# Optimization experiments

Measured on AMD Instinct MI355X. Metric: run time of the kernel, lower is better.

The kernel has to match this reference:

```python
import jax, jax.numpy as jnp
import numpy as np
from jax import lax

D_MODEL = 60
D_INNER = 120   # expand=2
D_STATE = 16
D_CONV = 4
DT_RANK = 4     # ceil(60/16)
DEPTH = 2
BATCH = 2
H_IMG = 128
W_IMG = 128
L_SEQ = H_IMG * W_IMG


def setup_inputs() -> dict:
    key = jax.random.key(0)
    ks = jax.random.split(key, 12)
    s = 0.02
    x = jax.random.normal(ks[0], (BATCH, L_SEQ, D_MODEL), jnp.float32)
    ln_w = jnp.ones((DEPTH, D_MODEL), jnp.float32)
    ln_b = jnp.zeros((DEPTH, D_MODEL), jnp.float32)
    in_proj_w = jax.random.normal(ks[1], (DEPTH, 2 * D_INNER, D_MODEL), jnp.float32) * s
    conv_w = jax.random.normal(ks[2], (DEPTH, D_INNER, D_CONV), jnp.float32) * s
    conv_b = jnp.zeros((DEPTH, D_INNER), jnp.float32)
    x_proj_w = jax.random.normal(ks[3], (DEPTH, DT_RANK + 2 * D_STATE, D_INNER), jnp.float32) * s
    dt_proj_w = jax.random.normal(ks[4], (DEPTH, D_INNER, DT_RANK), jnp.float32) * s
    dt_proj_b = jnp.full((DEPTH, D_INNER), -4.0, jnp.float32)  # softplus^-1 of small dt
    A_log = jnp.broadcast_to(
        jnp.log(jnp.arange(1, D_STATE + 1, dtype=jnp.float32))[None, None, :],
        (DEPTH, D_INNER, D_STATE)).copy()
    D_skip = jnp.ones((DEPTH, D_INNER), jnp.float32)
    out_proj_w = jax.random.normal(ks[5], (DEPTH, D_MODEL, D_INNER), jnp.float32) * s
    conv2d_w = jax.random.normal(ks[6], (D_MODEL, D_MODEL, 3, 3), jnp.float32) * s
    conv2d_b = jnp.zeros((D_MODEL,), jnp.float32)
    return {"x": x, "ln_w": ln_w, "ln_b": ln_b, "in_proj_w": in_proj_w,
            "conv_w": conv_w, "conv_b": conv_b, "x_proj_w": x_proj_w,
            "dt_proj_w": dt_proj_w, "dt_proj_b": dt_proj_b, "A_log": A_log,
            "D": D_skip, "out_proj_w": out_proj_w,
            "conv2d_w": conv2d_w, "conv2d_b": conv2d_b,
            "H": H_IMG, "W": W_IMG}


def _layernorm(x, w, b, eps=1e-5):
    mu = jnp.mean(x, axis=-1, keepdims=True)
    var = jnp.mean(jnp.square(x - mu), axis=-1, keepdims=True)
    return (x - mu) * lax.rsqrt(var + eps) * w + b


def _selective_scan(dA, dBx, C):
    # dA, dBx: [B, L, D_INNER, D_STATE]; C: [B, L, D_STATE]
    def step(h, inp):
        dA_t, dBx_t, c_t = inp
        h = dA_t * h + dBx_t                       # [B, D_INNER, D_STATE]
        y = jnp.einsum('bdn,bn->bd', h, c_t)
        return h, y
    h0 = jnp.zeros(dA.shape[:1] + dA.shape[2:], dA.dtype)
    _, ys = lax.scan(step, h0,
                     (dA.transpose(1, 0, 2, 3), dBx.transpose(1, 0, 2, 3),
                      C.transpose(1, 0, 2)))
    return ys.transpose(1, 0, 2)                    # [B, L, D_INNER]


def _mamba(x, in_w, cw, cb, xp_w, dtw, dtb, A_log, D_skip, out_w):
    # x: [B, L, D_MODEL]
    xz = jnp.einsum('bld,ed->ble', x, in_w)         # [B, L, 2*D_INNER]
    xin, z = jnp.split(xz, 2, axis=-1)
    # causal depthwise conv1d over L
    xc = xin.transpose(0, 2, 1)                     # [B, D_INNER, L]
    xc = jnp.pad(xc, ((0, 0), (0, 0), (D_CONV - 1, 0)))
    xc = lax.conv_general_dilated(xc, cw[:, None, :], (1,), 'VALID',
                                  dimension_numbers=('NCH', 'OIH', 'NCH'),
                                  feature_group_count=D_INNER)
    xc = jax.nn.silu(xc + cb[None, :, None]).transpose(0, 2, 1)  # [B, L, D_INNER]
    xdb = jnp.einsum('bld,ed->ble', xc, xp_w)       # [B, L, DT_RANK + 2*D_STATE]
    dt = xdb[..., :DT_RANK]
    Bm = xdb[..., DT_RANK:DT_RANK + D_STATE]
    Cm = xdb[..., DT_RANK + D_STATE:]
    delta = jax.nn.softplus(jnp.einsum('blr,dr->bld', dt, dtw) + dtb)  # [B, L, D_INNER]
    A = -jnp.exp(A_log)                              # [D_INNER, D_STATE]
    dA = jnp.exp(delta[..., None] * A[None, None])   # [B, L, D_INNER, D_STATE]
    dBx = delta[..., None] * Bm[:, :, None, :] * xc[..., None]
    y = _selective_scan(dA, dBx, Cm) + D_skip * xc
    y = y * jax.nn.silu(z)
    return jnp.einsum('ble,de->bld', y, out_w)       # [B, L, D_MODEL]


def reference(x, ln_w, ln_b, in_proj_w, conv_w, conv_b, x_proj_w,
              dt_proj_w, dt_proj_b, A_log, D, out_proj_w,
              conv2d_w, conv2d_b, H, W):
    h = x
    for i in range(DEPTH):
        hn = _layernorm(h, ln_w[i], ln_b[i])
        h = _mamba(hn, in_proj_w[i], conv_w[i], conv_b[i], x_proj_w[i],
                   dt_proj_w[i], dt_proj_b[i], A_log[i], D[i], out_proj_w[i])
    # patch_unembed -> 3x3 conv -> patch_embed, residual add (RMMB)
    b = h.shape[0]
    img = h.transpose(0, 2, 1).reshape(b, D_MODEL, H, W)
    img = lax.conv_general_dilated(img, conv2d_w, (1, 1), 'SAME',
                                   dimension_numbers=('NCHW', 'OIHW', 'NCHW'))
    img = img + conv2d_b[None, :, None, None]
    h = img.reshape(b, D_MODEL, H * W).transpose(0, 2, 1)
    return h + x
```

## Files before the change

kernel.cpp:

```cpp
#include <hip/hip_runtime.h>
#include <math.h>

#define BATCH 2
#define LSEQ 16384
#define DM 60
#define DI 120
#define NCH 512
#define TCH 32
#define HH 128
#define WW 128

typedef __attribute__((ext_vector_type(8))) short bhalf8;
typedef __attribute__((ext_vector_type(4))) short short4v;
typedef __attribute__((ext_vector_type(4))) float f32x4;

__device__ __forceinline__ float sigmoidf_(float x){ return __builtin_amdgcn_rcpf(1.0f + __expf(-x)); }
__device__ __forceinline__ float siluf_(float x){ return x * sigmoidf_(x); }
__device__ __forceinline__ float softplusf_(float x){ return (x > 20.0f) ? x : __logf(1.0f + __expf(x)); }
__device__ __forceinline__ short f2b(float f){
  union{float f; unsigned u;} v; v.f = f;
  unsigned r = (v.u + 0x7fffu + ((v.u >> 16) & 1u)) >> 16;
  return (short)r;
}
__device__ __forceinline__ float b2f(short s){
  union{float f; unsigned u;} v; v.u = ((unsigned)(unsigned short)s) << 16; return v.f;
}

__device__ __forceinline__ void powers16(float r, float* dA){
  dA[0] = r;
  #pragma unroll
  for (int n = 1; n < 16; n++) dA[n] = dA[(n-1)>>1] * dA[n>>1];
}
__device__ __forceinline__ void powers8(float r, float* p){
  p[0] = r;
  #pragma unroll
  for (int n = 1; n < 8; n++) p[n] = p[(n-1)>>1] * p[n>>1];
}

__global__ __launch_bounds__(256) void k_pack(
    const float* __restrict__ ipw, const float* __restrict__ xpw,
    const float* __restrict__ opw,
    const float* __restrict__ lnw, const float* __restrict__ lnb,
    short* __restrict__ pk, float* __restrict__ c01)
{
  int i = blockIdx.x*256 + threadIdx.x;
  if (i < 2*240*64){
    int l = i / (240*64);
    int rem = i % (240*64);
    int n = rem / 64, k = rem % 64;
    float v = (k < 60) ? ipw[(size_t)l*14400 + n*60 + k] * lnw[l*60 + k] : 0.f;
    pk[i] = f2b(v);
  } else if (i < 30720 + 2*48*128){
    int j = i - 30720;
    int l = j / (48*128);
    int rem = j % (48*128);
    int n = rem / 128, k = rem % 128;
    float v = (n < 36 && k < 120) ? xpw[(size_t)l*36*120 + n*120 + k] : 0.f;
    pk[i] = f2b(v);
  } else if (i < 43008 + 480){
    int j = i - 43008;
    int l = j / 240, n = j % 240;
    float c1 = 0.f, c0 = 0.f;
    for (int k = 0; k < 60; k++){
      float w = ipw[(size_t)l*14400 + n*60 + k];
      c1 += lnw[l*60+k] * w;
      c0 += lnb[l*60+k] * w;
    }
    c01[(l*240 + n)*2 + 0] = c1;
    c01[(l*240 + n)*2 + 1] = c0;
  } else if (i < 43488 + 2*64*128){
    int j = i - 43488;
    int l = j / 8192;
    int rem = j % 8192;
    int n = rem / 128, k = rem % 128;
    float v = (n < 60 && k < 120) ? opw[(size_t)l*7200 + n*120 + k] : 0.f;
    pk[43008 + j] = f2b(v);
  }
}

__global__ __launch_bounds__(512) void k_lnxp(
    const float* __restrict__ srcf, const short* __restrict__ srcb,
    const short* __restrict__ ipB,
    const float* __restrict__ c01,
    const float* __restrict__ cw, const float* __restrict__ cb,
    const short* __restrict__ xpB,
    const float* __restrict__ dtw, const float* __restrict__ dtb,
    const float* __restrict__ A_log,
    short* __restrict__ zs, short* __restrict__ xcg,
    short* __restrict__ delta, short* __restrict__ BCg,
    float* __restrict__ ap, float* __restrict__ he)
{
  __shared__ __align__(16) char smem[31552];
  short* XB   = (short*)smem;
  short* xcB  = (short*)smem;
  short* xinB = (short*)(smem + 8704);
  short* delL = (short*)(smem + 8704);
  float* BLf  = (float*)(smem + 21760);
  short* BCL  = (short*)(smem + 23808);
  float* stats= (float*)(smem + 25856);
  float* dtsh = (float*)(smem + 26240);
  float* cwL  = (float*)(smem + 26752);
  float* Wd5T = (float*)(smem + 28672);
  float* cbL  = (float*)(smem + 30592);
  float* bdL  = (float*)(smem + 31072);
  const int tid = threadIdx.x;
  const int wave = tid >> 6, lane = tid & 63;
  const int m = lane & 15, quad = lane >> 4;
  const int row0 = blockIdx.x * 32;
  const int seq0 = (row0 / LSEQ) * LSEQ;
  if (tid < 480){ cwL[tid] = cw[tid]; Wd5T[(tid & 3)*120 + (tid >> 2)] = dtw[tid]; }
  if (tid < 120){ cbL[tid] = cb[tid]; bdL[tid] = dtb[tid]; }
  for (int i = tid; i < 48*16; i += 512){
    int r = i >> 4, g = i & 15;
    int grow = row0 - 3 + r;
    short4v o = {0,0,0,0};
    if (g < 15 && r < 35 && grow >= seq0){
      if (srcb){
        o = *(const short4v*)&srcb[(size_t)grow*60 + g*4];
      } else {
        float4 f = *(const float4*)&srcf[(size_t)grow*60 + g*4];
        o.x = f2b(f.x); o.y = f2b(f.y); o.z = f2b(f.z); o.w = f2b(f.w);
      }
    }
    *(short4v*)&XB[r*72 + g*4] = o;
  }
  __syncthreads();
  {
    const int sub = lane >> 4;
    const int li  = lane & 15;
    #pragma unroll
    for (int it = 0; it < 2; it++){
      int r = it*32 + wave*4 + sub;
      if (r < 48){
        short4v x4 = *(const short4v*)&XB[r*72 + li*4];
        float f0 = b2f(x4.x), f1 = b2f(x4.y), f2 = b2f(x4.z), f3 = b2f(x4.w);
        float sx = (f0 + f1) + (f2 + f3);
        float sq = (f0*f0 + f1*f1) + (f2*f2 + f3*f3);
        #pragma unroll
        for (int off = 1; off < 16; off <<= 1){
          sx += __shfl_xor(sx, off);
          sq += __shfl_xor(sq, off);
        }
        if (li == 0){
          float mu = sx * (1.0f/60.0f);
          float var = fmaxf(sq * (1.0f/60.0f) - mu*mu, 0.f);
          stats[r*2 + 0] = mu;
          stats[r*2 + 1] = rsqrtf(var + 1e-5f);
        }
      }
    }
  }
  __syncthreads();
  for (int t = wave; t < 45; t += 8){
    int mtile = t / 15, ntile = t % 15;
    f32x4 acc = {0.f,0.f,0.f,0.f};
    #pragma unroll
    for (int ks = 0; ks < 2; ks++){
      bhalf8 a = *(const bhalf8*)&XB[(mtile*16 + m)*72 + ks*32 + quad*8];
      bhalf8 b = *(const bhalf8*)&ipB[(ntile*16 + m)*64 + ks*32 + quad*8];
      acc = __builtin_amdgcn_mfma_f32_16x16x32_bf16(a, b, acc, 0, 0, 0);
    }
    int n = ntile*16 + m;
    float2 cc = *(const float2*)&c01[n*2];
    float c1v = cc.x, c0v = cc.y;
    #pragma unroll
    for (int reg = 0; reg < 4; reg++){
      int r = mtile*16 + quad*4 + reg;
      int grow = row0 - 3 + r;
      bool valid = (r < 35) && (grow >= seq0);
      float mu = stats[r*2], rs = stats[r*2+1];
      float val = rs*(acc[reg] - mu*c1v) + c0v;
      if (!valid) val = 0.f;
      if (n < 120){
        xinB[r*136 + n] = f2b(val);
      } else if (r >= 3 && r < 35){
        zs[(size_t)(row0 - 3 + r)*120 + (n - 120)] = f2b(siluf_(val));
      }
    }
  }
  __syncthreads();
  for (int i = tid; i < 960; i += 512){
    int r = i/30, c4 = (i%30)*4;
    float4 cbv = *(const float4*)&cbL[c4];
    float4 w0 = *(const float4*)&cwL[(c4+0)*4];
    float4 w1 = *(const float4*)&cwL[(c4+1)*4];
    float4 w2 = *(const float4*)&cwL[(c4+2)*4];
    float4 w3 = *(const float4*)&cwL[(c4+3)*4];
    short4v x0 = *(const short4v*)&xinB[(r+0)*136 + c4];
    short4v x1 = *(const short4v*)&xinB[(r+1)*136 + c4];
    short4v x2 = *(const short4v*)&xinB[(r+2)*136 + c4];
    short4v x3 = *(const short4v*)&xinB[(r+3)*136 + c4];
    float a0 = cbv.x + w0.x*b2f(x0.x) + w0.y*b2f(x1.x) + w0.z*b2f(x2.x) + w0.w*b2f(x3.x);
    float a1 = cbv.y + w1.x*b2f(x0.y) + w1.y*b2f(x1.y) + w1.z*b2f(x2.y) + w1.w*b2f(x3.y);
    float a2 = cbv.z + w2.x*b2f(x0.z) + w2.y*b2f(x1.z) + w2.z*b2f(x2.z) + w2.w*b2f(x3.z);
    float a3 = cbv.w + w3.x*b2f(x0.w) + w3.y*b2f(x1.w) + w3.z*b2f(x2.w) + w3.w*b2f(x3.w);
    short4v o;
    o.x = f2b(siluf_(a0)); o.y = f2b(siluf_(a1)); o.z = f2b(siluf_(a2)); o.w = f2b(siluf_(a3));
    *(short4v*)&xcB[r*136 + c4] = o;
  }
  for (int i = tid; i < 32*8; i += 512)
    xcB[(i >> 3)*136 + 120 + (i & 7)] = 0;
  __syncthreads();
  for (int t = wave; t < 6; t += 8){
    int mtile = t / 3, ntile = t % 3;
    f32x4 acc = {0.f,0.f,0.f,0.f};
    #pragma unroll
    for (int ks = 0; ks < 4; ks++){
      bhalf8 a = *(const bhalf8*)&xcB[(mtile*16 + m)*136 + ks*32 + quad*8];
      bhalf8 b = *(const bhalf8*)&xpB[(ntile*16 + m)*128 + ks*32 + quad*8];
      acc = __builtin_amdgcn_mfma_f32_16x16x32_bf16(a, b, acc, 0, 0, 0);
    }
    int n = ntile*16 + m;
    #pragma unroll
    for (int reg = 0; reg < 4; reg++){
      int r = mtile*16 + quad*4 + reg;
      float val = acc[reg];
      if (n < 4)        dtsh[r*4 + n] = val;
      else if (n < 36){
        BCL[r*32 + (n - 4)] = f2b(val);
        if (n < 20) BLf[r*16 + (n - 4)] = val;
      }
    }
  }
  __syncthreads();
  for (int i = tid; i < 960; i += 512){
    int row = i/30, c4 = (i%30)*4;
    float4 t4 = *(const float4*)&dtsh[row*4];
    float4 w0 = *(const float4*)&Wd5T[0*120 + c4];
    float4 w1 = *(const float4*)&Wd5T[1*120 + c4];
    float4 w2 = *(const float4*)&Wd5T[2*120 + c4];
    float4 w3 = *(const float4*)&Wd5T[3*120 + c4];
    float4 bb = *(const float4*)&bdL[c4];
    short4v o;
    o.x = f2b(softplusf_(bb.x + t4.x*w0.x + t4.y*w1.x + t4.z*w2.x + t4.w*w3.x));
    o.y = f2b(softplusf_(bb.y + t4.x*w0.y + t4.y*w1.y + t4.z*w2.y + t4.w*w3.y));
    o.z = f2b(softplusf_(bb.z + t4.x*w0.z + t4.y*w1.z + t4.z*w2.z + t4.w*w3.z));
    o.w = f2b(softplusf_(bb.w + t4.x*w0.w + t4.y*w1.w + t4.z*w2.w + t4.w*w3.w));
    *(short4v*)&delL[row*120 + c4] = o;
    *(short4v*)&delta[(size_t)(row0 + row)*120 + c4] = o;
  }
  __syncthreads();
  for (int i = tid; i < 960; i += 512){
    int r = i/30, off = (i%30)*4;
    *(short4v*)&xcg[(size_t)(row0 + r)*120 + off] = *(const short4v*)&xcB[r*136 + off];
  }
  for (int i = tid; i < 256; i += 512)
    *(short4v*)&BCg[(size_t)row0*32 + i*4] = *(const short4v*)&BCL[i*4];
  if (tid < 480){
    const int d = tid >> 2, q = tid & 3, n0 = q << 2;
    const int b = row0 / LSEQ;
    const int cglob = (row0 % LSEQ) >> 5;
    float A2[4], h[4];
    const float A20 = -__expf(A_log[d*16]) * 1.44269504f;
    #pragma unroll
    for (int n = 0; n < 4; n++){
      A2[n] = -__expf(A_log[d*16 + n0 + n]) * 1.44269504f;
      h[n] = 0.f;
    }
    bool fastp = true;
    #pragma unroll
    for (int n = 0; n < 4; n++)
      fastp = fastp && (fabsf(A2[n] - (n0+n+1)*A20) <= 1e-4f*fabsf(A2[n]));
    int fp = fastp ? 1 : 0;
    fp &= __shfl_xor(fp, 1);
    fp &= __shfl_xor(fp, 2);
    int base = (cglob*BATCH + b)*(DI*16) + d*16 + n0;
    if (fp){
      float P = 1.f;
      const int sh1 = q & 1, sh2 = q & 2;
      for (int t = 0; t < 32; t++){
        float del = b2f(delL[t*120 + d]);
        float xcv = b2f(xcB[t*136 + d]);
        float dx = del * xcv;
        float r = exp2f(del * A20);
        P *= r;
        float p1 = r*r;
        float p2 = p1*r, p3 = p1*p1;
        float s = sh1 ? p3 : 1.0f;
        if (sh2) s *= p3*p3;
        float4 bv = *(const float4*)&BLf[t*16 + n0];
        h[0] = (s*r )*h[0] + dx*bv.x;
        h[1] = (s*p1)*h[1] + dx*bv.y;
        h[2] = (s*p2)*h[2] + dx*bv.z;
        h[3] = (s*p3)*h[3] + dx*bv.w;
      }
      float P1 = P*P;
      float P2 = P1*P, P3 = P1*P1;
      float sP = sh1 ? P3 : 1.0f;
      if (sh2) sP *= P3*P3;
      float apv[4] = {sP*P, sP*P1, sP*P2, sP*P3};
      *(float4*)&ap[base] = *(float4*)&apv[0];
      *(float4*)&he[base] = *(float4*)&h[0];
    } else {
      float apv[4] = {1.f,1.f,1.f,1.f};
      for (int t = 0; t < 32; t++){
        float del = b2f(delL[t*120 + d]);
        float dx = del * b2f(xcB[t*136 + d]);
        #pragma unroll
        for (int n = 0; n < 4; n++){
          float dA = exp2f(del * A2[n]);
          apv[n] *= dA;
          h[n] = dA*h[n] + dx*BLf[t*16 + n0 + n];
        }
      }
      *(float4*)&ap[base] = *(float4*)&apv[0];
      *(float4*)&he[base] = *(float4*)&h[0];
    }
  }
}

__global__ __launch_bounds__(256) void k_scan2(float* __restrict__ ap, const float* __restrict__ he)
{
  __shared__ float aggA[16*17];
  __shared__ float aggB[16*17];
  const int tid = threadIdx.x;
  const int n = tid & 15, j = tid >> 4;
  const int sbase = blockIdx.x*16 + n;
  const int stride = BATCH*DI*16;
  {
    float A = 1.f, B = 0.f;
    int idx = (j*32)*stride + sbase;
    #pragma unroll 4
    for (int k = 0; k < 32; k++){
      float a = ap[idx], h = he[idx];
      B = a*B + h;
      A *= a;
      idx += stride;
    }
    aggA[n*17 + j] = A;
    aggB[n*17 + j] = B;
  }
  __syncthreads();
  if (tid < 16){
    float B = 0.f;
    #pragma unroll
    for (int jj = 0; jj < 16; jj++){
      float Af = aggA[tid*17 + jj];
      float Bf = aggB[tid*17 + jj];
      aggB[tid*17 + jj] = B;
      B = Af*B + Bf;
    }
  }
  __syncthreads();
  {
    float H = aggB[n*17 + j];
    int idx = (j*32)*stride + sbase;
    #pragma unroll 4
    for (int k = 0; k < 32; k++){
      float a = ap[idx], h = he[idx];
      ap[idx] = H;
      H = a*H + h;
      idx += stride;
    }
  }
}

__global__ __launch_bounds__(256) void k_scan3o(
    const short* __restrict__ delta, const short* __restrict__ xc,
    const short* __restrict__ BCg, const short* __restrict__ zs,
    const float* __restrict__ h0, const float* __restrict__ A_log,
    const float* __restrict__ Dsk, const short* __restrict__ opB,
    short* __restrict__ hout)
{
  __shared__ float BCl[TCH*32];
  __shared__ __align__(16) short yL[TCH*136];
  const int tid = threadIdx.x;
  const int wave = tid >> 6, lane = tid & 63;
  const int m = lane & 15, quad = lane >> 4;
  const int c = blockIdx.x % NCH, b = blockIdx.x / NCH;
  const size_t rowbase = (size_t)b*LSEQ + (size_t)c*TCH;
  for (int i = tid; i < TCH*8; i += 256){
    short4v v = *(const short4v*)&BCg[rowbase*32 + i*4];
    float4 f; f.x = b2f(v.x); f.y = b2f(v.y); f.z = b2f(v.z); f.w = b2f(v.w);
    *(float4*)&BCl[i*4] = f;
  }
  for (int i = tid; i < TCH*4; i += 256){
    short4v z = {0,0,0,0};
    *(short4v*)&yL[(i >> 2)*136 + 120 + (i & 3)*4] = z;
  }
  __syncthreads();
  if (tid < 240){
    const int d = tid >> 1, half = tid & 1, n0 = half << 3;
    float A2[8], h[8];
    const int base = (c*BATCH + b)*(DI*16) + d*16 + n0;
    const float A20 = -__expf(A_log[d*16]) * 1.44269504f;
    #pragma unroll
    for (int n = 0; n < 8; n++){
      A2[n] = -__expf(A_log[d*16 + n0 + n]) * 1.44269504f;
      h[n] = h0[base + n];
    }
    bool fastp = true;
    #pragma unroll
    for (int n = 0; n < 8; n++)
      fastp = fastp && (fabsf(A2[n] - (n0+n+1)*A20) <= 1e-4f*fabsf(A2[n]));
    int fp = fastp ? 1 : 0;
    fp &= __shfl_xor(fp, 1);
    const float Dv = Dsk[d];
    if (fp){
      for (int t = 0; t < TCH; t++){
        float del = b2f(delta[(rowbase+t)*DI + d]);
        float xcv = b2f(xc[(rowbase+t)*DI + d]);
        float zv  = b2f(zs[(rowbase+t)*DI + d]);
        float dx = del * xcv;
        float r = exp2f(del * A20);
        float p8[8]; powers8(r, p8);
        float s = half ? p8[7] : 1.0f;
        float4 b0 = *(const float4*)&BCl[t*32 + n0];
        float4 b1 = *(const float4*)&BCl[t*32 + n0 + 4];
        h[0] = (s*p8[0])*h[0] + dx*b0.x;  h[1] = (s*p8[1])*h[1] + dx*b0.y;
        h[2] = (s*p8[2])*h[2] + dx*b0.z;  h[3] = (s*p8[3])*h[3] + dx*b0.w;
        h[4] = (s*p8[4])*h[4] + dx*b1.x;  h[5] = (s*p8[5])*h[5] + dx*b1.y;
        h[6] = (s*p8[6])*h[6] + dx*b1.z;  h[7] = (s*p8[7])*h[7] + dx*b1.w;
        float4 c0 = *(const float4*)&BCl[t*32 + 16 + n0];
        float4 c1 = *(const float4*)&BCl[t*32 + 20 + n0];
        float acc = h[0]*c0.x + h[1]*c0.y + h[2]*c0.z + h[3]*c0.w
                  + h[4]*c1.x + h[5]*c1.y + h[6]*c1.z + h[7]*c1.w;
        acc += __shfl_xor(acc, 1);
        if (!half) yL[t*136 + d] = f2b((acc + Dv*xcv) * zv);
      }
    } else {
      for (int t = 0; t < TCH; t++){
        float del = b2f(delta[(rowbase+t)*DI + d]);
        float xcv = b2f(xc[(rowbase+t)*DI + d]);
        float zv  = b2f(zs[(rowbase+t)*DI + d]);
        float dx = del * xcv;
        float acc = 0.f;
        #pragma unroll
        for (int n = 0; n < 8; n++){
          float dA = exp2f(del * A2[n]);
          h[n] = dA*h[n] + dx*BCl[t*32 + n0 + n];
          acc += h[n]*BCl[t*32 + 16 + n0 + n];
        }
        acc += __shfl_xor(acc, 1);
        if (!half) yL[t*136 + d] = f2b((acc + Dv*xcv) * zv);
      }
    }
  }
  __syncthreads();
  for (int t = wave; t < 8; t += 4){
    const int mtile = t >> 2, ntile = t & 3;
    f32x4 acc = {0.f,0.f,0.f,0.f};
    #pragma unroll
    for (int ks = 0; ks < 4; ks++){
      bhalf8 a  = *(const bhalf8*)&yL[(mtile*16 + m)*136 + ks*32 + quad*8];
      bhalf8 bb = *(const bhalf8*)&opB[(ntile*16 + m)*128 + ks*32 + quad*8];
      acc = __builtin_amdgcn_mfma_f32_16x16x32_bf16(a, bb, acc, 0, 0, 0);
    }
    const int n = ntile*16 + m;
    if (n < 60){
      #pragma unroll
      for (int reg = 0; reg < 4; reg++){
        int r = mtile*16 + quad*4 + reg;
        hout[(rowbase + r)*60 + n] = f2b(acc[reg]);
      }
    }
  }
}

__global__ __launch_bounds__(256) void k_wB(const float* __restrict__ w, short* __restrict__ wB)
{
  int i = blockIdx.x*256 + threadIdx.x;
  if (i >= 9*64*64) return;
  int ci = i & 63, co = (i >> 6) & 63, tap = i >> 12;
  float v = 0.f;
  if (co < 60 && ci < 60) v = w[((size_t)co*60 + ci)*9 + tap];
  wB[i] = f2b(v);
}

__global__ __launch_bounds__(256) void k_conv2d(
    const short* __restrict__ hin, const short* __restrict__ wB,
    const float* __restrict__ cb, const float* __restrict__ xres,
    float* __restrict__ out)
{
  __shared__ short tile[3*66*72];
  const int tid = threadIdx.x;
  const int blk = blockIdx.x;
  const int xhalf = blk & 1;
  const int yy = (blk >> 1) & 127;
  const int b = blk >> 8;
  const int x0 = xhalf*64;
  for (int i = tid; i < 3*66*18; i += 256){
    int g = i % 18;
    int xx = (i / 18) % 66;
    int row = i / (18*66);
    int gy = yy - 1 + row, gx = x0 - 1 + xx;
    short4v v = {0,0,0,0};
    if (g < 15 && gy >= 0 && gy < HH && gx >= 0 && gx < WW)
      v = *(const short4v*)&hin[((size_t)b*LSEQ + gy*WW + gx)*60 + g*4];
    *(short4v*)&tile[(row*66 + xx)*72 + g*4] = v;
  }
  __syncthreads();
  const int wave = tid >> 6, lane = tid & 63;
  const int m = lane & 15, quad = lane >> 4;
  f32x4 acc0 = {0.f,0.f,0.f,0.f}, acc1 = {0.f,0.f,0.f,0.f};
  f32x4 acc2 = {0.f,0.f,0.f,0.f}, acc3 = {0.f,0.f,0.f,0.f};
  #pragma unroll
  for (int tap = 0; tap < 9; tap++){
    const int ky = tap/3, kx = tap%3;
    const short* arow = &tile[(ky*66 + wave*16 + m + kx)*72];
    const short* brow = wB + tap*4096;
    #pragma unroll
    for (int kh = 0; kh < 2; kh++){
      const int k0 = kh*32 + quad*8;
      bhalf8 a = *(const bhalf8*)(arow + k0);
      bhalf8 b0 = *(const bhalf8*)(brow + (0*16 + m)*64 + k0);
      bhalf8 b1 = *(const bhalf8*)(brow + (1*16 + m)*64 + k0);
      bhalf8 b2 = *(const bhalf8*)(brow + (2*16 + m)*64 + k0);
      bhalf8 b3 = *(const bhalf8*)(brow + (3*16 + m)*64 + k0);
      acc0 = __builtin_amdgcn_mfma_f32_16x16x32_bf16(a, b0, acc0, 0, 0, 0);
      acc1 = __builtin_amdgcn_mfma_f32_16x16x32_bf16(a, b1, acc1, 0, 0, 0);
      acc2 = __builtin_amdgcn_mfma_f32_16x16x32_bf16(a, b2, acc2, 0, 0, 0);
      acc3 = __builtin_amdgcn_mfma_f32_16x16x32_bf16(a, b3, acc3, 0, 0, 0);
    }
  }
  const size_t rowb = (size_t)b*LSEQ + yy*WW + x0;
  f32x4 accs[4] = {acc0, acc1, acc2, acc3};
  #pragma unroll
  for (int nt = 0; nt < 4; nt++){
    int co = nt*16 + m;
    if (co < 60){
      float bias = cb[co];
      #pragma unroll
      for (int reg = 0; reg < 4; reg++){
        int px = wave*16 + quad*4 + reg;
        size_t o = (rowb + px)*60 + co;
        out[o] = accs[nt][reg] + bias + xres[o];
      }
    }
  }
}

extern "C" void kernel_launch(void* const* d_in, const int* in_sizes, int n_in,
                              void* d_out, int out_size, void* d_ws, size_t ws_size,
                              hipStream_t stream)
{
  const float* x      = (const float*)d_in[0];
  const float* ln_w   = (const float*)d_in[1];
  const float* ln_b   = (const float*)d_in[2];
  const float* ipw    = (const float*)d_in[3];
  const float* cw     = (const float*)d_in[4];
  const float* cb1    = (const float*)d_in[5];
  const float* xpw    = (const float*)d_in[6];
  const float* dtw    = (const float*)d_in[7];
  const float* dtb    = (const float*)d_in[8];
  const float* A_log  = (const float*)d_in[9];
  const float* Dsk    = (const float*)d_in[10];
  const float* opw    = (const float*)d_in[11];
  const float* c2w    = (const float*)d_in[12];
  const float* c2b    = (const float*)d_in[13];
  float* out = (float*)d_out;

  char* ws = (char*)d_ws;
  size_t off = 0;
  short* zsb   = (short*)(ws + off); off += (size_t)BATCH*LSEQ*DI*2;
  short* xcb   = (short*)(ws + off); off += (size_t)BATCH*LSEQ*DI*2;
  short* dlt   = (short*)(ws + off); off += (size_t)BATCH*LSEQ*DI*2;
  short* BCg   = (short*)(ws + off); off += (size_t)BATCH*LSEQ*32*2;
  float* apb   = (float*)(ws + off); off += (size_t)NCH*BATCH*DI*16*4;
  float* heb   = (float*)(ws + off); off += (size_t)NCH*BATCH*DI*16*4;
  short* hcur  = (short*)(ws + off); off += (size_t)BATCH*LSEQ*DM*2;
  short* wBb   = (short*)(ws + off); off += (size_t)9*64*64*2;
  short* pkb   = (short*)(ws + off); off += (size_t)(2*240*64 + 2*48*128 + 2*64*128)*2;
  float* c01b  = (float*)(ws + off); off += (size_t)2*240*2*4;

  const int rows = BATCH*LSEQ;
  k_pack<<<(43008 + 480 + 16384 + 255)/256, 256, 0, stream>>>(ipw, xpw, opw, ln_w, ln_b, pkb, c01b);
  for (int layer = 0; layer < 2; layer++){
    const float* srcf = (layer == 0) ? x : nullptr;
    const short* srcb = (layer == 0) ? nullptr : hcur;
    k_lnxp<<<rows/32, 512, 0, stream>>>(srcf, srcb,
                                        pkb + (size_t)layer*240*64,
                                        c01b + (size_t)layer*240*2,
                                        cw + layer*DI*4, cb1 + layer*DI,
                                        pkb + 30720 + (size_t)layer*48*128,
                                        dtw + (size_t)layer*DI*4, dtb + layer*DI,
                                        A_log + (size_t)layer*DI*16,
                                        zsb, xcb, dlt, BCg, apb, heb);
    k_scan2<<<BATCH*DI, 256, 0, stream>>>(apb, heb);
    k_scan3o<<<BATCH*NCH, 256, 0, stream>>>(dlt, xcb, BCg, zsb, apb, A_log + (size_t)layer*DI*16,
                                            Dsk + layer*DI, pkb + 43008 + (size_t)layer*8192, hcur);
  }
  k_wB<<<(9*64*64+255)/256, 256, 0, stream>>>(c2w, wBb);
  k_conv2d<<<BATCH*HH*2, 256, 0, stream>>>(hcur, wBb, c2b, x, out);
}
```

Baseline: 277.6 us.

## Stage scan inputs in LDS and unroll chunk-state scan two steps

In k_scan3o, delta, xc and z for the chunk are now loaded cooperatively with vectorized loads into shared memory before the sequential scan. Previously each scan step issued scattered 2-byte global loads. In k_lnxp, fp32 copies of delta and the convolved x are kept in LDS so the chunk-state pass skips bf16 conversions. That pass is also unrolled by two timesteps, combining decays to shorten the dependent chain. This grows LDS usage (k_lnxp to about 48KB), which may lower occupancy.

```diff
diff --git a/kernel.cpp b/kernel.cpp
--- a/kernel.cpp
+++ b/kernel.cpp
@@ -26,11 +26,6 @@
   union{float f; unsigned u;} v; v.u = ((unsigned)(unsigned short)s) << 16; return v.f;
 }
 
-__device__ __forceinline__ void powers16(float r, float* dA){
-  dA[0] = r;
-  #pragma unroll
-  for (int n = 1; n < 16; n++) dA[n] = dA[(n-1)>>1] * dA[n>>1];
-}
 __device__ __forceinline__ void powers8(float r, float* p){
   p[0] = r;
   #pragma unroll
@@ -90,19 +85,20 @@
     short* __restrict__ delta, short* __restrict__ BCg,
     float* __restrict__ ap, float* __restrict__ he)
 {
-  __shared__ __align__(16) char smem[31552];
+  __shared__ __align__(16) char smem[49216];
   short* XB   = (short*)smem;
   short* xcB  = (short*)smem;
   short* xinB = (short*)(smem + 8704);
-  short* delL = (short*)(smem + 8704);
-  float* BLf  = (float*)(smem + 21760);
-  short* BCL  = (short*)(smem + 23808);
-  float* stats= (float*)(smem + 25856);
-  float* dtsh = (float*)(smem + 26240);
-  float* cwL  = (float*)(smem + 26752);
-  float* Wd5T = (float*)(smem + 28672);
-  float* cbL  = (float*)(smem + 30592);
-  float* bdL  = (float*)(smem + 31072);
+  float* delLf= (float*)(smem + 8704);
+  float* xcf  = (float*)(smem + 24064);
+  float* BLf  = (float*)(smem + 39424);
+  short* BCL  = (short*)(smem + 41472);
+  float* stats= (float*)(smem + 43520);
+  float* dtsh = (float*)(smem + 43904);
+  float* cwL  = (float*)(smem + 44416);
+  float* Wd5T = (float*)(smem + 46336);
+  float* cbL  = (float*)(smem + 48256);
+  float* bdL  = (float*)(smem + 48736);
   const int tid = threadIdx.x;
   const int wave = tid >> 6, lane = tid & 63;
   const int m = lane & 15, quad = lane >> 4;
@@ -194,8 +190,11 @@
     float a1 = cbv.y + w1.x*b2f(x0.y) + w1.y*b2f(x1.y) + w1.z*b2f(x2.y) + w1.w*b2f(x3.y);
     float a2 = cbv.z + w2.x*b2f(x0.z) + w2.y*b2f(x1.z) + w2.z*b2f(x2.z) + w2.w*b2f(x3.z);
     float a3 = cbv.w + w3.x*b2f(x0.w) + w3.y*b2f(x1.w) + w3.z*b2f(x2.w) + w3.w*b2f(x3.w);
+    a0 = siluf_(a0); a1 = siluf_(a1); a2 = siluf_(a2); a3 = siluf_(a3);
+    float4 fo; fo.x = a0; fo.y = a1; fo.z = a2; fo.w = a3;
+    *(float4*)&xcf[r*120 + c4] = fo;
     short4v o;
-    o.x = f2b(siluf_(a0)); o.y = f2b(siluf_(a1)); o.z = f2b(siluf_(a2)); o.w = f2b(siluf_(a3));
+    o.x = f2b(a0); o.y = f2b(a1); o.z = f2b(a2); o.w = f2b(a3);
     *(short4v*)&xcB[r*136 + c4] = o;
   }
   for (int i = tid; i < 32*8; i += 512)
@@ -231,12 +230,14 @@
     float4 w2 = *(const float4*)&Wd5T[2*120 + c4];
     float4 w3 = *(const float4*)&Wd5T[3*120 + c4];
     float4 bb = *(const float4*)&bdL[c4];
+    float4 dd;
+    dd.x = softplusf_(bb.x + t4.x*w0.x + t4.y*w1.x + t4.z*w2.x + t4.w*w3.x);
+    dd.y = softplusf_(bb.y + t4.x*w0.y + t4.y*w1.y + t4.z*w2.y + t4.w*w3.y);
+    dd.z = softplusf_(bb.z + t4.x*w0.z + t4.y*w1.z + t4.z*w2.z + t4.w*w3.z);
+    dd.w = softplusf_(bb.w + t4.x*w0.w + t4.y*w1.w + t4.z*w2.w + t4.w*w3.w);
+    *(float4*)&delLf[row*120 + c4] = dd;
     short4v o;
-    o.x = f2b(softplusf_(bb.x + t4.x*w0.x + t4.y*w1.x + t4.z*w2.x + t4.w*w3.x));
-    o.y = f2b(softplusf_(bb.y + t4.x*w0.y + t4.y*w1.y + t4.z*w2.y + t4.w*w3.y));
-    o.z = f2b(softplusf_(bb.z + t4.x*w0.z + t4.y*w1.z + t4.z*w2.z + t4.w*w3.z));
-    o.w = f2b(softplusf_(bb.w + t4.x*w0.w + t4.y*w1.w + t4.z*w2.w + t4.w*w3.w));
-    *(short4v*)&delL[row*120 + c4] = o;
+    o.x = f2b(dd.x); o.y = f2b(dd.y); o.z = f2b(dd.z); o.w = f2b(dd.w);
     *(short4v*)&delta[(size_t)(row0 + row)*120 + c4] = o;
   }
   __syncthreads();
@@ -264,25 +265,31 @@
     int fp = fastp ? 1 : 0;
     fp &= __shfl_xor(fp, 1);
     fp &= __shfl_xor(fp, 2);
+    const int sh1 = q & 1, sh2 = q & 2;
     int base = (cglob*BATCH + b)*(DI*16) + d*16 + n0;
     if (fp){
       float P = 1.f;
-      const int sh1 = q & 1, sh2 = q & 2;
-      for (int t = 0; t < 32; t++){
-        float del = b2f(delL[t*120 + d]);
-        float xcv = b2f(xcB[t*136 + d]);
-        float dx = del * xcv;
-        float r = exp2f(del * A20);
-        P *= r;
-        float p1 = r*r;
-        float p2 = p1*r, p3 = p1*p1;
-        float s = sh1 ? p3 : 1.0f;
-        if (sh2) s *= p3*p3;
-        float4 bv = *(const float4*)&BLf[t*16 + n0];
-        h[0] = (s*r )*h[0] + dx*bv.x;
-        h[1] = (s*p1)*h[1] + dx*bv.y;
-        h[2] = (s*p2)*h[2] + dx*bv.z;
-        h[3] = (s*p3)*h[3] + dx*bv.w;
+      for (int t = 0; t < 32; t += 2){
+        float d1 = delLf[t*120 + d],     d2 = delLf[(t+1)*120 + d];
+        float x1 = xcf[t*120 + d],       x2 = xcf[(t+1)*120 + d];
+        float dx1 = d1*x1, dx2 = d2*x2;
+        float r2s = exp2f(d2*A20);
+        float rr  = exp2f((d1+d2)*A20);
+        P *= rr;
+        float c1 = rr*rr, c2 = c1*rr, c3 = c1*c1;
+        float sc = sh1 ? c3 : 1.0f; if (sh2) sc *= c3*c3;
+        float p1 = r2s*r2s, p2 = p1*r2s, p3 = p1*p1;
+        float s2 = sh1 ? p3 : 1.0f; if (sh2) s2 *= p3*p3;
+        float4 b1 = *(const float4*)&BLf[t*16 + n0];
+        float4 b2 = *(const float4*)&BLf[(t+1)*16 + n0];
+        float ad0 = (s2*r2s)*dx1*b1.x + dx2*b2.x;
+        float ad1 = (s2*p1 )*dx1*b1.y + dx2*b2.y;
+        float ad2 = (s2*p2 )*dx1*b1.z + dx2*b2.z;
+        float ad3 = (s2*p3 )*dx1*b1.w + dx2*b2.w;
+        h[0] = (sc*rr)*h[0] + ad0;
+        h[1] = (sc*c1)*h[1] + ad1;
+        h[2] = (sc*c2)*h[2] + ad2;
+        h[3] = (sc*c3)*h[3] + ad3;
       }
       float P1 = P*P;
       float P2 = P1*P, P3 = P1*P1;
@@ -294,8 +301,8 @@
     } else {
       float apv[4] = {1.f,1.f,1.f,1.f};
       for (int t = 0; t < 32; t++){
-        float del = b2f(delL[t*120 + d]);
-        float dx = del * b2f(xcB[t*136 + d]);
+        float del = delLf[t*120 + d];
+        float dx = del * xcf[t*120 + d];
         #pragma unroll
         for (int n = 0; n < 4; n++){
           float dA = exp2f(del * A2[n]);
@@ -364,11 +371,20 @@
 {
   __shared__ float BCl[TCH*32];
   __shared__ __align__(16) short yL[TCH*136];
+  __shared__ __align__(16) short dL[TCH*120];
+  __shared__ __align__(16) short xL[TCH*120];
+  __shared__ __align__(16) short zL[TCH*120];
   const int tid = threadIdx.x;
   const int wave = tid >> 6, lane = tid & 63;
   const int m = lane & 15, quad = lane >> 4;
   const int c = blockIdx.x % NCH, b = blockIdx.x / NCH;
   const size_t rowbase = (size_t)b*LSEQ + (size_t)c*TCH;
+  for (int i = tid; i < 960; i += 256)
+    *(short4v*)&dL[i*4] = *(const short4v*)&delta[rowbase*DI + i*4];
+  for (int i = tid; i < 960; i += 256)
+    *(short4v*)&xL[i*4] = *(const short4v*)&xc[rowbase*DI + i*4];
+  for (int i = tid; i < 960; i += 256)
+    *(short4v*)&zL[i*4] = *(const short4v*)&zs[rowbase*DI + i*4];
   for (int i = tid; i < TCH*8; i += 256){
     short4v v = *(const short4v*)&BCg[rowbase*32 + i*4];
     float4 f; f.x = b2f(v.x); f.y = b2f(v.y); f.z = b2f(v.z); f.w = b2f(v.w);
@@ -398,9 +414,9 @@
     const float Dv = Dsk[d];
     if (fp){
       for (int t = 0; t < TCH; t++){
-        float del = b2f(delta[(rowbase+t)*DI + d]);
-        float xcv = b2f(xc[(rowbase+t)*DI + d]);
-        float zv  = b2f(zs[(rowbase+t)*DI + d]);
+        float del = b2f(dL[t*120 + d]);
+        float xcv = b2f(xL[t*120 + d]);
+        float zv  = b2f(zL[t*120 + d]);
         float dx = del * xcv;
         float r = exp2f(del * A20);
         float p8[8]; powers8(r, p8);
@@ -420,9 +436,9 @@
       }
     } else {
       for (int t = 0; t < TCH; t++){
-        float del = b2f(delta[(rowbase+t)*DI + d]);
-        float xcv = b2f(xc[(rowbase+t)*DI + d]);
-        float zv  = b2f(zs[(rowbase+t)*DI + d]);
+        float del = b2f(dL[t*120 + d]);
+        float xcv = b2f(xL[t*120 + d]);
+        float zv  = b2f(zL[t*120 + d]);
         float dx = del * xcv;
         float acc = 0.f;
         #pragma unroll
```

New measurement: 257.8 us. -7.1%, faster.
